# Performance work log

Hardware: AMD Instinct MI355X
Metric: run time of the kernel (lower is better)

The kernel has to match this reference:

```python
import jax, jax.numpy as jnp
import numpy as np

N = 8192        # n_nodes
NFEAT = 512
NHID = 256
AVG_DEG = 32
K = 64          # mean_kwargs k
TEMP = 1.0      # mean_kwargs temperature


def setup_inputs() -> dict:
    key = jax.random.key(0)
    ks = jax.random.split(key, 5)
    x = jax.random.normal(ks[0], (N, NFEAT), jnp.float32)
    edge_index = jax.random.randint(ks[1], (2, N * AVG_DEG), 0, N, dtype=jnp.int64)
    W1 = jax.random.normal(ks[2], (NFEAT, NHID), jnp.float32) / np.sqrt(NFEAT)
    b1 = jnp.zeros((NHID,), jnp.float32)
    W2 = jax.random.normal(ks[3], (NHID, NHID), jnp.float32) / np.sqrt(NHID)
    b2 = jnp.zeros((NHID,), jnp.float32)
    return {"x": x, "edge_index": edge_index, "W1": W1, "b1": b1, "W2": W2, "b2": b2}


def _gcn_norm(edge_index, n, dtype):
    # PyG gcn_norm: add self-loops (weight 1), deg over col, sym normalization
    loops = jnp.arange(n, dtype=edge_index.dtype)
    row = jnp.concatenate([edge_index[0], loops])
    col = jnp.concatenate([edge_index[1], loops])
    w = jnp.ones(row.shape[0], dtype)
    deg = jnp.zeros((n,), dtype).at[col].add(w)
    dis = jnp.where(deg > 0, jax.lax.rsqrt(jnp.where(deg > 0, deg, 1.0)), 0.0)
    return row, col, dis[row] * w * dis[col]


def _soft_k_medoid(row, col, w, x):
    # soft_weighted_medoid_k_neighborhood(A, x, k=K, temperature=TEMP, with_weight_correction=True)
    n, d = x.shape
    A = jnp.zeros((n, n), x.dtype).at[row, col].add(w)   # coalesced dense adjacency
    topk_a, topk_idx = jax.lax.top_k(A, K)               # [n, K] neighbor weights / ids
    xk = x[topk_idx]                                     # [n, K, d]
    sq = jnp.sum(xk * xk, axis=-1)                       # [n, K]
    G = jnp.einsum('nkd,nld->nkl', xk, xk)               # Gram per node
    d2 = jnp.maximum(sq[:, :, None] + sq[:, None, :] - 2.0 * G, 0.0)
    pos = d2 > 0
    dist = jnp.where(pos, jnp.sqrt(jnp.where(pos, d2, 1.0)), 0.0)  # safe sqrt (grad-safe)
    # weighted sum of distances to each top-k candidate j: c[n,j] = sum_l a[n,l] * ||x_l - x_j||
    c = jnp.einsum('nl,nlj->nj', topk_a, dist)
    c = jnp.where(topk_a == 0, jnp.finfo(x.dtype).max, c)
    soft = jax.nn.softmax(-c / TEMP, axis=-1)            # [n, K]
    soft = soft * topk_a                                 # with_weight_correction
    soft = soft / jnp.sum(soft, axis=-1, keepdims=True)
    row_sum = jnp.sum(A, axis=-1)                        # preserve neighborhood mass
    return row_sum[:, None] * jnp.einsum('nk,nkd->nd', soft, xk)


def reference(x, edge_index, W1, b1, W2, b2):
    n = x.shape[0]
    row, col, w = _gcn_norm(edge_index, n, x.dtype)
    h = jax.nn.relu(_soft_k_medoid(row, col, w, x @ W1) + b1)   # gc1 + relu (dropout: eval = identity)
    return jax.nn.relu(_soft_k_medoid(row, col, w, h @ W2) + b2)  # gc2 + relu
```

## Files before the change

### kernel.cpp

```cpp
#include <hip/hip_runtime.h>

typedef _Float16 half4 __attribute__((ext_vector_type(4)));
typedef _Float16 half8 __attribute__((ext_vector_type(8)));
typedef float f32x4 __attribute__((ext_vector_type(4)));

#define NNODE 8192
#define NHID  256
#define RCAP  128
#define KCAP  64

__global__ __launch_bounds__(256) void k_fused1(
    int* deg, int* rowcnt, int* flag, const void* edges,
    const float* __restrict__ W1, _Float16* __restrict__ w1T,
    const float* __restrict__ W2, _Float16* __restrict__ w2T,
    const float* __restrict__ x, _Float16* __restrict__ xh) {
    const int b = blockIdx.x, t = threadIdx.x;
    if (b < 32) {
        int i = b * 256 + t;
        deg[i] = 0; rowcnt[i] = 0;
        if (i == 0) {
            const long long* e = (const long long*)edges;
            int ok = 1;
            for (int k = 0; k < 64; ++k) { long long v = e[k]; if (v < 0 || v >= NNODE) ok = 0; }
            *flag = ok;
        }
    } else if (b < 32 + 4096) {
        int i = (b - 32) * 256 + t;
        float4 v = ((const float4*)x)[i];
        half4 h;
        h[0] = (_Float16)v.x; h[1] = (_Float16)v.y;
        h[2] = (_Float16)v.z; h[3] = (_Float16)v.w;
        *(half4*)&xh[4 * (size_t)i] = h;
    } else if (b < 32 + 4096 + 512) {
        int idx = (b - 4128) * 256 + t;
        int k = idx >> 8, n = idx & 255;
        w1T[(size_t)n * 512 + k] = (_Float16)W1[idx];
    } else {
        int idx = (b - 4640) * 256 + t;
        int k = idx >> 8, n = idx & 255;
        w2T[(size_t)n * 256 + k] = (_Float16)W2[idx];
    }
}

#define GLS 72

__device__ __forceinline__ void gemm_body(
    const _Float16* __restrict__ Ahi, const _Float16* __restrict__ BT,
    _Float16* __restrict__ Chi, int K, int bm, int bn) {
    __shared__ _Float16 sA[64][GLS];
    __shared__ _Float16 sB[64][GLS];
    const int t = threadIdx.x;
    const int lane = t & 63, L15 = lane & 15, q = lane >> 4;
    const int w = t >> 6, wr = w >> 1, wc = w & 1;
    f32x4 acc[2][2];
#pragma unroll
    for (int a = 0; a < 2; ++a)
#pragma unroll
        for (int b2 = 0; b2 < 2; ++b2) acc[a][b2] = (f32x4){0.f, 0.f, 0.f, 0.f};

    for (int k0 = 0; k0 < K; k0 += 64) {
#pragma unroll
        for (int i = 0; i < 2; ++i) {
            int row = i * 32 + (t >> 3), ch = t & 7;
            *(half8*)&sA[row][ch * 8] =
                *(const half8*)(Ahi + (size_t)(bm + row) * K + k0 + ch * 8);
            *(half8*)&sB[row][ch * 8] =
                *(const half8*)(BT + (size_t)(bn + row) * K + k0 + ch * 8);
        }
        __syncthreads();
#pragma unroll
        for (int ks = 0; ks < 2; ++ks) {
            const int ko = ks * 32 + q * 8;
            half8 ah[2], bh[2];
#pragma unroll
            for (int tr = 0; tr < 2; ++tr)
                ah[tr] = *(const half8*)&sA[32 * wr + 16 * tr + L15][ko];
#pragma unroll
            for (int tc = 0; tc < 2; ++tc)
                bh[tc] = *(const half8*)&sB[32 * wc + 16 * tc + L15][ko];
#pragma unroll
            for (int tr = 0; tr < 2; ++tr)
#pragma unroll
                for (int tc = 0; tc < 2; ++tc)
                    acc[tr][tc] = __builtin_amdgcn_mfma_f32_16x16x32_f16(ah[tr], bh[tc], acc[tr][tc], 0, 0, 0);
        }
        __syncthreads();
    }
#pragma unroll
    for (int tr = 0; tr < 2; ++tr)
#pragma unroll
        for (int tc = 0; tc < 2; ++tc)
#pragma unroll
            for (int r = 0; r < 4; ++r) {
                int rowg = bm + 32 * wr + 16 * tr + q * 4 + r;
                int colg = bn + 32 * wc + 16 * tc + L15;
                Chi[(size_t)rowg * NHID + colg] = (_Float16)acc[tr][tc][r];
            }
}

__global__ __launch_bounds__(256) void k_fused2(
    const void* edges, const int* flag, int* rowcnt, int* nbr, int* deg, int E, int nbuild,
    const _Float16* __restrict__ xh, const _Float16* __restrict__ w1T, _Float16* __restrict__ X1) {
    if ((int)blockIdx.x < nbuild) {
        int i = blockIdx.x * 256 + threadIdx.x;
        int total = E + NNODE;
        if (i >= total) return;
        int r, c;
        if (i < E) {
            if (*flag) {
                const long long* e = (const long long*)edges;
                r = (int)e[i]; c = (int)e[E + i];
            } else {
                const int* e = (const int*)edges;
                r = e[i]; c = e[E + i];
            }
        } else { r = i - E; c = r; }
        int pos = atomicAdd(&rowcnt[r], 1);
        if (pos < RCAP) nbr[r * RCAP + pos] = c;
        atomicAdd(&deg[c], 1);
    } else {
        int g = blockIdx.x - nbuild;
        gemm_body(xh, w1T, X1, 512, (g >> 2) * 64, (g & 3) * 64);
    }
}

__global__ __launch_bounds__(256) void k_gemm(
    const _Float16* __restrict__ Ahi, const _Float16* __restrict__ BT,
    _Float16* __restrict__ Chi, int K) {
    gemm_body(Ahi, BT, Chi, K, blockIdx.x * 64, blockIdx.y * 64);
}

__global__ __launch_bounds__(256) void k_dedup(const int* __restrict__ nbr,
                                               const int* __restrict__ rowcnt,
                                               const int* __restrict__ deg,
                                               int* __restrict__ cols,
                                               float* __restrict__ wout,
                                               float* __restrict__ rsum) {
    __shared__ int lc[2][RCAP];
    __shared__ float lw[2][RCAP];
    __shared__ unsigned char kp[2][RCAP];
    __shared__ int s_cw[2][2];
    __shared__ float s_rw[2][2];
    const int t = threadIdx.x;
    const int half = t >> 7, st = t & 127;
    const int wid = st >> 6, lane = t & 63;
    const int r = blockIdx.x * 2 + half;
    int n = rowcnt[r]; if (n > RCAP) n = RCAP;
    if (st < n) lc[half][st] = nbr[r * RCAP + st];
    __syncthreads();
    float dr = 1.f / sqrtf((float)deg[r]);
    bool keep = false; float wv = 0.f;
    if (st < n) {
        int c = lc[half][st];
        int mult = 0; bool first = true;
        for (int i = 0; i < n; ++i) {
            int ci = lc[half][i];
            if (ci == c) { mult++; if (i < st) first = false; }
        }
        keep = first;
        if (first) wv = (float)mult * dr * (1.f / sqrtf((float)deg[c]));
    }
    kp[half][st] = keep ? 1 : 0; lw[half][st] = wv;
    float rv = wv;
#pragma unroll
    for (int d = 1; d < 64; d <<= 1) rv += __shfl_xor(rv, d, 64);
    unsigned long long b = __ballot(keep);
    int pre = __popcll(b & ((1ull << lane) - 1ull));
    int cw = __popcll(b);
    if (lane == 0) { s_cw[half][wid] = cw; s_rw[half][wid] = rv; }
    __syncthreads();
    int total = s_cw[half][0] + s_cw[half][1];
    if (st == 0) rsum[r] = s_rw[half][0] + s_rw[half][1];
    const int base = r * KCAP;
    if (total <= KCAP) {
        int off = (wid ? s_cw[half][0] : 0) + pre;
        if (keep) { cols[base + off] = lc[half][st]; wout[base + off] = wv; }
        for (int m = total + st; m < KCAP; m += 128) { cols[base + m] = r; wout[base + m] = 0.f; }
    } else if (st == 0) {
        for (int s = 0; s < KCAP; ++s) {
            int best = -1;
            for (int i = 0; i < n; ++i) {
                if (!kp[half][i]) continue;
                if (best < 0 || lw[half][i] > lw[half][best] ||
                    (lw[half][i] == lw[half][best] && lc[half][i] < lc[half][best])) best = i;
            }
            cols[base + s] = lc[half][best]; wout[base + s] = lw[half][best]; kp[half][best] = 0;
        }
    }
}

#define SK 136

__global__ __launch_bounds__(256, 6) void k_medoid(
    const _Float16* __restrict__ Xhi,
    const float* __restrict__ bias,
    float* __restrict__ OutF, _Float16* __restrict__ OutHi,
    const int* __restrict__ cols, const float* __restrict__ wts,
    const float* __restrict__ rsum, int writeH) {
    __shared__ _Float16 sh[64][SK];
    __shared__ float s_a[64];
    __shared__ float s_sq[64];
    __shared__ float s_cpart[2][64];
    __shared__ float s_u[64];
    __shared__ int   s_cols[64];
    __shared__ float s_red[4][288];

    const int node = blockIdx.x;
    const int t = threadIdx.x;
    const int w = t >> 6, lane = t & 63;
    const int L15 = lane & 15, q = lane >> 4;
    const int wr = w >> 1, wc = w & 1;

    if (t < 64) { s_cols[t] = cols[node * KCAP + t]; s_a[t] = wts[node * KCAP + t]; }
    __syncthreads();

    f32x4 acc[2][2];
#pragma unroll
    for (int a = 0; a < 2; ++a)
#pragma unroll
        for (int b = 0; b < 2; ++b) acc[a][b] = (f32x4){0.f, 0.f, 0.f, 0.f};

    const int ch = t & 15, rr = t >> 4;
    for (int phase = 0; phase < 2; ++phase) {
#pragma unroll
        for (int i = 0; i < 4; ++i) {
            int l = i * 16 + rr;
            *(half8*)&sh[l][ch * 8] =
                *(const half8*)(Xhi + ((size_t)s_cols[l] << 8) + phase * 128 + ch * 8);
        }
        __syncthreads();
#pragma unroll
        for (int ks = 0; ks < 4; ++ks) {
            const int ko = ks * 32 + q * 8;
            half8 ah[2], bh[2];
#pragma unroll
            for (int tr = 0; tr < 2; ++tr) ah[tr] = *(const half8*)&sh[32 * wr + 16 * tr + L15][ko];
#pragma unroll
            for (int tc = 0; tc < 2; ++tc) bh[tc] = *(const half8*)&sh[32 * wc + 16 * tc + L15][ko];
#pragma unroll
            for (int tr = 0; tr < 2; ++tr)
#pragma unroll
                for (int tc = 0; tc < 2; ++tc)
                    acc[tr][tc] = __builtin_amdgcn_mfma_f32_16x16x32_f16(ah[tr], bh[tc], acc[tr][tc], 0, 0, 0);
        }
        if (phase == 0) __syncthreads();
    }

#pragma unroll
    for (int tr = 0; tr < 2; ++tr)
#pragma unroll
        for (int tc = 0; tc < 2; ++tc)
            if (32 * wr + 16 * tr == 32 * wc + 16 * tc) {
#pragma unroll
                for (int r = 0; r < 4; ++r)
                    if (L15 == q * 4 + r) s_sq[32 * wr + 16 * tr + L15] = acc[tr][tc][r];
            }
    __syncthreads();

    f32x4 sq4[2], a4[2];
#pragma unroll
    for (int tr = 0; tr < 2; ++tr) {
        sq4[tr] = *(const f32x4*)&s_sq[32 * wr + 16 * tr + 4 * q];
        a4[tr]  = *(const f32x4*)&s_a [32 * wr + 16 * tr + 4 * q];
    }
#pragma unroll
    for (int tc = 0; tc < 2; ++tc) {
        const int colg = 32 * wc + 16 * tc + L15;
        const float sqc = s_sq[colg];
        float pj = 0.f;
#pragma unroll
        for (int tr = 0; tr < 2; ++tr)
#pragma unroll
            for (int r = 0; r < 4; ++r) {
                float d2 = sq4[tr][r] + sqc - 2.f * acc[tr][tc][r];
                float dist = d2 > 0.f ? __builtin_amdgcn_sqrtf(d2) : 0.f;
                pj = fmaf(a4[tr][r], dist, pj);
            }
        pj += __shfl_xor(pj, 16, 64);
        pj += __shfl_xor(pj, 32, 64);
        if (q == 0) s_cpart[wr][colg] = pj;
    }
    __syncthreads();

    if (w == 0) {
        int j = lane;
        float c = s_cpart[0][j] + s_cpart[1][j];
        float aj = s_a[j];
        bool valid = aj > 0.f;
        float cv = valid ? c : 3.4e38f;
        float mn = cv;
#pragma unroll
        for (int d = 1; d < 64; d <<= 1) mn = fminf(mn, __shfl_xor(mn, d, 64));
        float e = valid ? __expf(mn - c) * aj : 0.f;
        float s = e;
#pragma unroll
        for (int d = 1; d < 64; d <<= 1) s += __shfl_xor(s, d, 64);
        s_u[j] = e * (rsum[node] / s);
    }
    __syncthreads();

    const int oct = t & 31, jb = t >> 5;
    float accd[8] = {0.f, 0.f, 0.f, 0.f, 0.f, 0.f, 0.f, 0.f};
#pragma unroll
    for (int jj = 0; jj < 8; ++jj) {
        int j = jb * 8 + jj;
        float u = s_u[j];
        half8 xv;
        if (oct < 16) xv = *(const half8*)(Xhi + ((size_t)s_cols[j] << 8) + oct * 8);
        else          xv = *(const half8*)&sh[j][(oct - 16) * 8];
#pragma unroll
        for (int e = 0; e < 8; ++e) accd[e] = fmaf(u, (float)xv[e], accd[e]);
    }
#pragma unroll
    for (int e = 0; e < 8; ++e) accd[e] += __shfl_xor(accd[e], 32, 64);
    if (lane < 32) {
#pragma unroll
        for (int e = 0; e < 8; ++e) s_red[w][9 * oct + e] = accd[e];
    }
    __syncthreads();
    const int idx = 9 * (t >> 3) + (t & 7);
    float o = s_red[0][idx] + s_red[1][idx] + s_red[2][idx] + s_red[3][idx];
    float res = fmaxf(o + bias[t], 0.f);
    size_t oi = (size_t)node * NHID + t;
    if (writeH) OutHi[oi] = (_Float16)res;
    else        OutF[oi] = res;
}

extern "C" void kernel_launch(void* const* d_in, const int* in_sizes, int n_in,
                              void* d_out, int out_size, void* d_ws, size_t ws_size,
                              hipStream_t stream) {
    const float* x  = (const float*)d_in[0];
    const void*  ei = d_in[1];
    const float* W1 = (const float*)d_in[2];
    const float* b1 = (const float*)d_in[3];
    const float* W2 = (const float*)d_in[4];
    const float* b2 = (const float*)d_in[5];
    float* out = (float*)d_out;
    const int E = in_sizes[1] / 2;

    char* p = (char*)d_ws;
    auto alloc = [&](size_t bytes) { char* q = p; p += (bytes + 255) & ~(size_t)255; return q; };
    int*      deg    = (int*)alloc((size_t)NNODE * 4);
    int*      rowcnt = (int*)alloc((size_t)NNODE * 4);
    int*      flag   = (int*)alloc(256);
    int*      colsA  = (int*)alloc((size_t)NNODE * KCAP * 4);
    float*    wA     = (float*)alloc((size_t)NNODE * KCAP * 4);
    float*    rsum   = (float*)alloc((size_t)NNODE * 4);
    _Float16* xh     = (_Float16*)alloc((size_t)NNODE * 512 * 2);
    _Float16* w1T    = (_Float16*)alloc((size_t)512 * NHID * 2);
    _Float16* w2T    = (_Float16*)alloc((size_t)NHID * NHID * 2);
    _Float16* X1hi   = (_Float16*)alloc((size_t)NNODE * NHID * 2);
    _Float16* Hhi    = (_Float16*)alloc((size_t)NNODE * NHID * 2);
    int*      nbr    = (int*)alloc((size_t)NNODE * RCAP * 4);

    const int nbuild = (E + NNODE + 255) / 256;

    k_fused1<<<32 + 4096 + 512 + 256, 256, 0, stream>>>(deg, rowcnt, flag, ei, W1, w1T, W2, w2T, x, xh);
    k_fused2<<<nbuild + 512, 256, 0, stream>>>(ei, flag, rowcnt, nbr, deg, E, nbuild, xh, w1T, X1hi);
    k_dedup<<<NNODE / 2, 256, 0, stream>>>(nbr, rowcnt, deg, colsA, wA, rsum);
    k_medoid<<<NNODE, 256, 0, stream>>>(X1hi, b1, nullptr, Hhi, colsA, wA, rsum, 1);
    k_gemm<<<dim3(NNODE / 64, NHID / 64), 256, 0, stream>>>(Hhi, w2T, X1hi, 256);
    k_medoid<<<NNODE, 256, 0, stream>>>(X1hi, b2, out, nullptr, colsA, wA, rsum, 0);
}
```

Before: 214.6 us.

## Merge all stages into one cooperative persistent kernel with grid syncs

```diff
diff --git a/kernel.cpp b/kernel.cpp
--- a/kernel.cpp
+++ b/kernel.cpp
@@ -1,4 +1,7 @@
 #include <hip/hip_runtime.h>
+#include <hip/hip_cooperative_groups.h>
+
+namespace cg = cooperative_groups;
 
 typedef _Float16 half4 __attribute__((ext_vector_type(4)));
 typedef _Float16 half8 __attribute__((ext_vector_type(8)));
@@ -8,47 +11,20 @@
 #define NHID  256
 #define RCAP  128
 #define KCAP  64
-
-__global__ __launch_bounds__(256) void k_fused1(
-    int* deg, int* rowcnt, int* flag, const void* edges,
-    const float* __restrict__ W1, _Float16* __restrict__ w1T,
-    const float* __restrict__ W2, _Float16* __restrict__ w2T,
-    const float* __restrict__ x, _Float16* __restrict__ xh) {
-    const int b = blockIdx.x, t = threadIdx.x;
-    if (b < 32) {
-        int i = b * 256 + t;
-        deg[i] = 0; rowcnt[i] = 0;
-        if (i == 0) {
-            const long long* e = (const long long*)edges;
-            int ok = 1;
-            for (int k = 0; k < 64; ++k) { long long v = e[k]; if (v < 0 || v >= NNODE) ok = 0; }
-            *flag = ok;
-        }
-    } else if (b < 32 + 4096) {
-        int i = (b - 32) * 256 + t;
-        float4 v = ((const float4*)x)[i];
-        half4 h;
-        h[0] = (_Float16)v.x; h[1] = (_Float16)v.y;
-        h[2] = (_Float16)v.z; h[3] = (_Float16)v.w;
-        *(half4*)&xh[4 * (size_t)i] = h;
-    } else if (b < 32 + 4096 + 512) {
-        int idx = (b - 4128) * 256 + t;
-        int k = idx >> 8, n = idx & 255;
-        w1T[(size_t)n * 512 + k] = (_Float16)W1[idx];
-    } else {
-        int idx = (b - 4640) * 256 + t;
-        int k = idx >> 8, n = idx & 255;
-        w2T[(size_t)n * 256 + k] = (_Float16)W2[idx];
-    }
-}
-
-#define GLS 72
+#define GLS   72
+#define SK    136
+
+struct SmemGemm   { _Float16 sA[64][GLS]; _Float16 sB[64][GLS]; };
+struct SmemDedup  { int lc[2][RCAP]; float lw[2][RCAP]; unsigned char kp[2][RCAP];
+                    int s_cw[2][2]; float s_rw[2][2]; };
+struct SmemMedoid { _Float16 sh[64][SK]; float s_a[64]; float s_sq[64];
+                    float s_cpart[2][64]; float s_u[64]; int s_cols[64];
+                    float s_red[4][288]; };
 
 __device__ __forceinline__ void gemm_body(
-    const _Float16* __restrict__ Ahi, const _Float16* __restrict__ BT,
+    char* smraw, const _Float16* __restrict__ Ahi, const _Float16* __restrict__ BT,
     _Float16* __restrict__ Chi, int K, int bm, int bn) {
-    __shared__ _Float16 sA[64][GLS];
-    __shared__ _Float16 sB[64][GLS];
+    SmemGemm& sm = *(SmemGemm*)smraw;
     const int t = threadIdx.x;
     const int lane = t & 63, L15 = lane & 15, q = lane >> 4;
     const int w = t >> 6, wr = w >> 1, wc = w & 1;
@@ -62,9 +38,9 @@
 #pragma unroll
         for (int i = 0; i < 2; ++i) {
             int row = i * 32 + (t >> 3), ch = t & 7;
-            *(half8*)&sA[row][ch * 8] =
+            *(half8*)&sm.sA[row][ch * 8] =
                 *(const half8*)(Ahi + (size_t)(bm + row) * K + k0 + ch * 8);
-            *(half8*)&sB[row][ch * 8] =
+            *(half8*)&sm.sB[row][ch * 8] =
                 *(const half8*)(BT + (size_t)(bn + row) * K + k0 + ch * 8);
         }
         __syncthreads();
@@ -74,10 +50,10 @@
             half8 ah[2], bh[2];
 #pragma unroll
             for (int tr = 0; tr < 2; ++tr)
-                ah[tr] = *(const half8*)&sA[32 * wr + 16 * tr + L15][ko];
+                ah[tr] = *(const half8*)&sm.sA[32 * wr + 16 * tr + L15][ko];
 #pragma unroll
             for (int tc = 0; tc < 2; ++tc)
-                bh[tc] = *(const half8*)&sB[32 * wc + 16 * tc + L15][ko];
+                bh[tc] = *(const half8*)&sm.sB[32 * wc + 16 * tc + L15][ko];
 #pragma unroll
             for (int tr = 0; tr < 2; ++tr)
 #pragma unroll
@@ -98,120 +74,72 @@
             }
 }
 
-__global__ __launch_bounds__(256) void k_fused2(
-    const void* edges, const int* flag, int* rowcnt, int* nbr, int* deg, int E, int nbuild,
-    const _Float16* __restrict__ xh, const _Float16* __restrict__ w1T, _Float16* __restrict__ X1) {
-    if ((int)blockIdx.x < nbuild) {
-        int i = blockIdx.x * 256 + threadIdx.x;
-        int total = E + NNODE;
-        if (i >= total) return;
-        int r, c;
-        if (i < E) {
-            if (*flag) {
-                const long long* e = (const long long*)edges;
-                r = (int)e[i]; c = (int)e[E + i];
-            } else {
-                const int* e = (const int*)edges;
-                r = e[i]; c = e[E + i];
-            }
-        } else { r = i - E; c = r; }
-        int pos = atomicAdd(&rowcnt[r], 1);
-        if (pos < RCAP) nbr[r * RCAP + pos] = c;
-        atomicAdd(&deg[c], 1);
-    } else {
-        int g = blockIdx.x - nbuild;
-        gemm_body(xh, w1T, X1, 512, (g >> 2) * 64, (g & 3) * 64);
-    }
-}
-
-__global__ __launch_bounds__(256) void k_gemm(
-    const _Float16* __restrict__ Ahi, const _Float16* __restrict__ BT,
-    _Float16* __restrict__ Chi, int K) {
-    gemm_body(Ahi, BT, Chi, K, blockIdx.x * 64, blockIdx.y * 64);
-}
-
-__global__ __launch_bounds__(256) void k_dedup(const int* __restrict__ nbr,
-                                               const int* __restrict__ rowcnt,
-                                               const int* __restrict__ deg,
-                                               int* __restrict__ cols,
-                                               float* __restrict__ wout,
-                                               float* __restrict__ rsum) {
-    __shared__ int lc[2][RCAP];
-    __shared__ float lw[2][RCAP];
-    __shared__ unsigned char kp[2][RCAP];
-    __shared__ int s_cw[2][2];
-    __shared__ float s_rw[2][2];
+__device__ __forceinline__ void dedup_body(
+    char* smraw, const int* __restrict__ nbr, const int* __restrict__ rowcnt,
+    const int* __restrict__ deg, int* __restrict__ cols, float* __restrict__ wout,
+    float* __restrict__ rsum, int grp) {
+    SmemDedup& sm = *(SmemDedup*)smraw;
     const int t = threadIdx.x;
     const int half = t >> 7, st = t & 127;
     const int wid = st >> 6, lane = t & 63;
-    const int r = blockIdx.x * 2 + half;
+    const int r = grp * 2 + half;
     int n = rowcnt[r]; if (n > RCAP) n = RCAP;
-    if (st < n) lc[half][st] = nbr[r * RCAP + st];
+    if (st < n) sm.lc[half][st] = nbr[r * RCAP + st];
     __syncthreads();
     float dr = 1.f / sqrtf((float)deg[r]);
     bool keep = false; float wv = 0.f;
     if (st < n) {
-        int c = lc[half][st];
+        int c = sm.lc[half][st];
         int mult = 0; bool first = true;
         for (int i = 0; i < n; ++i) {
-            int ci = lc[half][i];
+            int ci = sm.lc[half][i];
             if (ci == c) { mult++; if (i < st) first = false; }
         }
         keep = first;
         if (first) wv = (float)mult * dr * (1.f / sqrtf((float)deg[c]));
     }
-    kp[half][st] = keep ? 1 : 0; lw[half][st] = wv;
+    sm.kp[half][st] = keep ? 1 : 0; sm.lw[half][st] = wv;
     float rv = wv;
 #pragma unroll
     for (int d = 1; d < 64; d <<= 1) rv += __shfl_xor(rv, d, 64);
     unsigned long long b = __ballot(keep);
     int pre = __popcll(b & ((1ull << lane) - 1ull));
     int cw = __popcll(b);
-    if (lane == 0) { s_cw[half][wid] = cw; s_rw[half][wid] = rv; }
-    __syncthreads();
-    int total = s_cw[half][0] + s_cw[half][1];
-    if (st == 0) rsum[r] = s_rw[half][0] + s_rw[half][1];
+    if (lane == 0) { sm.s_cw[half][wid] = cw; sm.s_rw[half][wid] = rv; }
+    __syncthreads();
+    int total = sm.s_cw[half][0] + sm.s_cw[half][1];
+    if (st == 0) rsum[r] = sm.s_rw[half][0] + sm.s_rw[half][1];
     const int base = r * KCAP;
     if (total <= KCAP) {
-        int off = (wid ? s_cw[half][0] : 0) + pre;
-        if (keep) { cols[base + off] = lc[half][st]; wout[base + off] = wv; }
+        int off = (wid ? sm.s_cw[half][0] : 0) + pre;
+        if (keep) { cols[base + off] = sm.lc[half][st]; wout[base + off] = wv; }
         for (int m = total + st; m < KCAP; m += 128) { cols[base + m] = r; wout[base + m] = 0.f; }
     } else if (st == 0) {
         for (int s = 0; s < KCAP; ++s) {
             int best = -1;
             for (int i = 0; i < n; ++i) {
-                if (!kp[half][i]) continue;
-                if (best < 0 || lw[half][i] > lw[half][best] ||
-                    (lw[half][i] == lw[half][best] && lc[half][i] < lc[half][best])) best = i;
+                if (!sm.kp[half][i]) continue;
+                if (best < 0 || sm.lw[half][i] > sm.lw[half][best] ||
+                    (sm.lw[half][i] == sm.lw[half][best] && sm.lc[half][i] < sm.lc[half][best])) best = i;
             }
-            cols[base + s] = lc[half][best]; wout[base + s] = lw[half][best]; kp[half][best] = 0;
-        }
-    }
-}
-
-#define SK 136
-
-__global__ __launch_bounds__(256, 6) void k_medoid(
-    const _Float16* __restrict__ Xhi,
-    const float* __restrict__ bias,
+            cols[base + s] = sm.lc[half][best]; wout[base + s] = sm.lw[half][best]; sm.kp[half][best] = 0;
+        }
+    }
+    __syncthreads();
+}
+
+__device__ __forceinline__ void medoid_body(
+    char* smraw, const _Float16* __restrict__ Xhi, const float* __restrict__ bias,
     float* __restrict__ OutF, _Float16* __restrict__ OutHi,
     const int* __restrict__ cols, const float* __restrict__ wts,
-    const float* __restrict__ rsum, int writeH) {
-    __shared__ _Float16 sh[64][SK];
-    __shared__ float s_a[64];
-    __shared__ float s_sq[64];
-    __shared__ float s_cpart[2][64];
-    __shared__ float s_u[64];
-    __shared__ int   s_cols[64];
-    __shared__ float s_red[4][288];
-
-    const int node = blockIdx.x;
+    const float* __restrict__ rsum, int node, int writeH) {
+    SmemMedoid& sm = *(SmemMedoid*)smraw;
     const int t = threadIdx.x;
     const int w = t >> 6, lane = t & 63;
     const int L15 = lane & 15, q = lane >> 4;
     const int wr = w >> 1, wc = w & 1;
 
-    if (t < 64) { s_cols[t] = cols[node * KCAP + t]; s_a[t] = wts[node * KCAP + t]; }
+    if (t < 64) { sm.s_cols[t] = cols[node * KCAP + t]; sm.s_a[t] = wts[node * KCAP + t]; }
     __syncthreads();
 
     f32x4 acc[2][2];
@@ -225,8 +153,8 @@
 #pragma unroll
         for (int i = 0; i < 4; ++i) {
             int l = i * 16 + rr;
-            *(half8*)&sh[l][ch * 8] =
-                *(const half8*)(Xhi + ((size_t)s_cols[l] << 8) + phase * 128 + ch * 8);
+            *(half8*)&sm.sh[l][ch * 8] =
+                *(const half8*)(Xhi + ((size_t)sm.s_cols[l] << 8) + phase * 128 + ch * 8);
         }
         __syncthreads();
 #pragma unroll
@@ -234,9 +162,9 @@
             const int ko = ks * 32 + q * 8;
             half8 ah[2], bh[2];
 #pragma unroll
-            for (int tr = 0; tr < 2; ++tr) ah[tr] = *(const half8*)&sh[32 * wr + 16 * tr + L15][ko];
-#pragma unroll
-            for (int tc = 0; tc < 2; ++tc) bh[tc] = *(const half8*)&sh[32 * wc + 16 * tc + L15][ko];
+            for (int tr = 0; tr < 2; ++tr) ah[tr] = *(const half8*)&sm.sh[32 * wr + 16 * tr + L15][ko];
+#pragma unroll
+            for (int tc = 0; tc < 2; ++tc) bh[tc] = *(const half8*)&sm.sh[32 * wc + 16 * tc + L15][ko];
 #pragma unroll
             for (int tr = 0; tr < 2; ++tr)
 #pragma unroll
@@ -253,20 +181,20 @@
             if (32 * wr + 16 * tr == 32 * wc + 16 * tc) {
 #pragma unroll
                 for (int r = 0; r < 4; ++r)
-                    if (L15 == q * 4 + r) s_sq[32 * wr + 16 * tr + L15] = acc[tr][tc][r];
+                    if (L15 == q * 4 + r) sm.s_sq[32 * wr + 16 * tr + L15] = acc[tr][tc][r];
             }
     __syncthreads();
 
     f32x4 sq4[2], a4[2];
 #pragma unroll
     for (int tr = 0; tr < 2; ++tr) {
-        sq4[tr] = *(const f32x4*)&s_sq[32 * wr + 16 * tr + 4 * q];
-        a4[tr]  = *(const f32x4*)&s_a [32 * wr + 16 * tr + 4 * q];
+        sq4[tr] = *(const f32x4*)&sm.s_sq[32 * wr + 16 * tr + 4 * q];
+        a4[tr]  = *(const f32x4*)&sm.s_a [32 * wr + 16 * tr + 4 * q];
     }
 #pragma unroll
     for (int tc = 0; tc < 2; ++tc) {
         const int colg = 32 * wc + 16 * tc + L15;
-        const float sqc = s_sq[colg];
+        const float sqc = sm.s_sq[colg];
         float pj = 0.f;
 #pragma unroll
         for (int tr = 0; tr < 2; ++tr)
@@ -278,14 +206,14 @@
             }
         pj += __shfl_xor(pj, 16, 64);
         pj += __shfl_xor(pj, 32, 64);
-        if (q == 0) s_cpart[wr][colg] = pj;
+        if (q == 0) sm.s_cpart[wr][colg] = pj;
     }
     __syncthreads();
 
     if (w == 0) {
         int j = lane;
-        float c = s_cpart[0][j] + s_cpart[1][j];
-        float aj = s_a[j];
+        float c = sm.s_cpart[0][j] + sm.s_cpart[1][j];
+        float aj = sm.s_a[j];
         bool valid = aj > 0.f;
         float cv = valid ? c : 3.4e38f;
         float mn = cv;
@@ -295,7 +223,7 @@
         float s = e;
 #pragma unroll
         for (int d = 1; d < 64; d <<= 1) s += __shfl_xor(s, d, 64);
-        s_u[j] = e * (rsum[node] / s);
+        sm.s_u[j] = e * (rsum[node] / s);
     }
     __syncthreads();
 
@@ -304,10 +232,10 @@
 #pragma unroll
     for (int jj = 0; jj < 8; ++jj) {
         int j = jb * 8 + jj;
-        float u = s_u[j];
+        float u = sm.s_u[j];
         half8 xv;
-        if (oct < 16) xv = *(const half8*)(Xhi + ((size_t)s_cols[j] << 8) + oct * 8);
-        else          xv = *(const half8*)&sh[j][(oct - 16) * 8];
+        if (oct < 16) xv = *(const half8*)(Xhi + ((size_t)sm.s_cols[j] << 8) + oct * 8);
+        else          xv = *(const half8*)&sm.sh[j][(oct - 16) * 8];
 #pragma unroll
         for (int e = 0; e < 8; ++e) accd[e] = fmaf(u, (float)xv[e], accd[e]);
     }
@@ -315,15 +243,147 @@
     for (int e = 0; e < 8; ++e) accd[e] += __shfl_xor(accd[e], 32, 64);
     if (lane < 32) {
 #pragma unroll
-        for (int e = 0; e < 8; ++e) s_red[w][9 * oct + e] = accd[e];
+        for (int e = 0; e < 8; ++e) sm.s_red[w][9 * oct + e] = accd[e];
     }
     __syncthreads();
     const int idx = 9 * (t >> 3) + (t & 7);
-    float o = s_red[0][idx] + s_red[1][idx] + s_red[2][idx] + s_red[3][idx];
+    float o = sm.s_red[0][idx] + sm.s_red[1][idx] + sm.s_red[2][idx] + sm.s_red[3][idx];
     float res = fmaxf(o + bias[t], 0.f);
     size_t oi = (size_t)node * NHID + t;
     if (writeH) OutHi[oi] = (_Float16)res;
     else        OutF[oi] = res;
+}
+
+__device__ __forceinline__ void stage_prep(
+    int gid, int nthr, int bid, int t,
+    int* deg, int* rowcnt, int* flag, const void* edges,
+    const float* __restrict__ x, _Float16* __restrict__ xh,
+    const float* __restrict__ W1, _Float16* __restrict__ w1T,
+    const float* __restrict__ W2, _Float16* __restrict__ w2T) {
+    for (int i = gid; i < NNODE; i += nthr) { deg[i] = 0; rowcnt[i] = 0; }
+    if (bid == 0 && t < 64) {
+        const long long* e = (const long long*)edges;
+        long long v = e[t];
+        unsigned long long bad = __ballot(v < 0 || v >= (long long)NNODE);
+        if (t == 0) *flag = (bad == 0) ? 1 : 0;
+    }
+    for (int i = gid; i < NNODE * 512 / 4; i += nthr) {
+        float4 v = ((const float4*)x)[i];
+        half4 h;
+        h[0] = (_Float16)v.x; h[1] = (_Float16)v.y;
+        h[2] = (_Float16)v.z; h[3] = (_Float16)v.w;
+        *(half4*)&xh[4 * (size_t)i] = h;
+    }
+    for (int i = gid; i < 512 * NHID; i += nthr) {
+        int k = i >> 8, n = i & 255;
+        w1T[(size_t)n * 512 + k] = (_Float16)W1[i];
+    }
+    for (int i = gid; i < NHID * NHID; i += nthr) {
+        int k = i >> 8, n = i & 255;
+        w2T[(size_t)n * 256 + k] = (_Float16)W2[i];
+    }
+}
+
+__device__ __forceinline__ void stage_s1(
+    char* smem, int bid, int nb, int t,
+    const void* edges, const int* flag, int* rowcnt, int* nbr, int* deg, int E,
+    const _Float16* __restrict__ xh, const _Float16* __restrict__ w1T, _Float16* __restrict__ X1) {
+    const int ng = nb >> 1;
+    if (bid < ng) {
+        for (int g = bid; g < 512; g += ng)
+            gemm_body(smem, xh, w1T, X1, 512, (g >> 2) * 64, (g & 3) * 64);
+    } else {
+        const int ns = nb - ng;
+        const int fl = *flag;
+        const int total = E + NNODE;
+        for (int i = (bid - ng) * 256 + t; i < total; i += ns * 256) {
+            int r, c;
+            if (i < E) {
+                if (fl) {
+                    const long long* e = (const long long*)edges;
+                    r = (int)e[i]; c = (int)e[E + i];
+                } else {
+                    const int* e = (const int*)edges;
+                    r = e[i]; c = e[E + i];
+                }
+            } else { r = i - E; c = r; }
+            int pos = atomicAdd(&rowcnt[r], 1);
+            if (pos < RCAP) nbr[r * RCAP + pos] = c;
+            atomicAdd(&deg[c], 1);
+        }
+    }
+}
+
+__global__ __launch_bounds__(256, 4) void k_mega(
+    const float* __restrict__ x, const void* edges,
+    const float* __restrict__ W1, const float* __restrict__ b1,
+    const float* __restrict__ W2, const float* __restrict__ b2,
+    float* __restrict__ out,
+    int* deg, int* rowcnt, int* flag, int* nbr, int* cols, float* wA,
+    float* rsum, _Float16* xh, _Float16* w1T, _Float16* w2T,
+    _Float16* X1, _Float16* Hh, int E) {
+    cg::grid_group grid = cg::this_grid();
+    __shared__ __align__(16) char smem[sizeof(SmemMedoid)];
+    const int nb = gridDim.x, bid = blockIdx.x, t = threadIdx.x;
+    const int gid = bid * 256 + t, nthr = nb * 256;
+
+    stage_prep(gid, nthr, bid, t, deg, rowcnt, flag, edges, x, xh, W1, w1T, W2, w2T);
+    grid.sync();
+    stage_s1(smem, bid, nb, t, edges, flag, rowcnt, nbr, deg, E, xh, w1T, X1);
+    grid.sync();
+    for (int g = bid; g < NNODE / 2; g += nb)
+        dedup_body(smem, nbr, rowcnt, deg, cols, wA, rsum, g);
+    grid.sync();
+    for (int node = bid; node < NNODE; node += nb)
+        medoid_body(smem, X1, b1, nullptr, Hh, cols, wA, rsum, node, 1);
+    grid.sync();
+    for (int g = bid; g < 512; g += nb)
+        gemm_body(smem, Hh, w2T, X1, 256, (g >> 2) * 64, (g & 3) * 64);
+    grid.sync();
+    for (int node = bid; node < NNODE; node += nb)
+        medoid_body(smem, X1, b2, out, nullptr, cols, wA, rsum, node, 0);
+}
+
+__global__ __launch_bounds__(256) void fb_prep(
+    int* deg, int* rowcnt, int* flag, const void* edges,
+    const float* __restrict__ x, _Float16* __restrict__ xh,
+    const float* __restrict__ W1, _Float16* __restrict__ w1T,
+    const float* __restrict__ W2, _Float16* __restrict__ w2T) {
+    stage_prep(blockIdx.x * 256 + threadIdx.x, gridDim.x * 256, blockIdx.x, threadIdx.x,
+               deg, rowcnt, flag, edges, x, xh, W1, w1T, W2, w2T);
+}
+
+__global__ __launch_bounds__(256) void fb_s1(
+    const void* edges, const int* flag, int* rowcnt, int* nbr, int* deg, int E,
+    const _Float16* __restrict__ xh, const _Float16* __restrict__ w1T, _Float16* __restrict__ X1) {
+    __shared__ __align__(16) char smem[sizeof(SmemGemm)];
+    stage_s1(smem, blockIdx.x, gridDim.x, threadIdx.x, edges, flag, rowcnt, nbr, deg, E, xh, w1T, X1);
+}
+
+__global__ __launch_bounds__(256) void fb_dedup(
+    const int* __restrict__ nbr, const int* __restrict__ rowcnt, const int* __restrict__ deg,
+    int* __restrict__ cols, float* __restrict__ wout, float* __restrict__ rsum) {
+    __shared__ __align__(16) char smem[sizeof(SmemDedup)];
+    for (int g = blockIdx.x; g < NNODE / 2; g += gridDim.x)
+        dedup_body(smem, nbr, rowcnt, deg, cols, wout, rsum, g);
+}
+
+__global__ __launch_bounds__(256, 4) void fb_medoid(
+    const _Float16* __restrict__ Xhi, const float* __restrict__ bias,
+    float* __restrict__ OutF, _Float16* __restrict__ OutHi,
+    const int* __restrict__ cols, const float* __restrict__ wts,
+    const float* __restrict__ rsum, int writeH) {
+    __shared__ __align__(16) char smem[sizeof(SmemMedoid)];
+    for (int node = blockIdx.x; node < NNODE; node += gridDim.x)
+        medoid_body(smem, Xhi, bias, OutF, OutHi, cols, wts, rsum, node, writeH);
+}
+
+__global__ __launch_bounds__(256) void fb_gemm(
+    const _Float16* __restrict__ Ahi, const _Float16* __restrict__ BT,
+    _Float16* __restrict__ Chi, int K) {
+    __shared__ __align__(16) char smem[sizeof(SmemGemm)];
+    for (int g = blockIdx.x; g < 512; g += gridDim.x)
+        gemm_body(smem, Ahi, BT, Chi, K, (g >> 2) * 64, (g & 3) * 64);
 }
 
 extern "C" void kernel_launch(void* const* d_in, const int* in_sizes, int n_in,
@@ -336,7 +396,7 @@
     const float* W2 = (const float*)d_in[4];
     const float* b2 = (const float*)d_in[5];
     float* out = (float*)d_out;
-    const int E = in_sizes[1] / 2;
+    int E = in_sizes[1] / 2;
 
     char* p = (char*)d_ws;
     auto alloc = [&](size_t bytes) { char* q = p; p += (bytes + 255) & ~(size_t)255; return q; };
@@ -349,16 +409,41 @@
     _Float16* xh     = (_Float16*)alloc((size_t)NNODE * 512 * 2);
     _Float16* w1T    = (_Float16*)alloc((size_t)512 * NHID * 2);
     _Float16* w2T    = (_Float16*)alloc((size_t)NHID * NHID * 2);
-    _Float16* X1hi   = (_Float16*)alloc((size_t)NNODE * NHID * 2);
-    _Float16* Hhi    = (_Float16*)alloc((size_t)NNODE * NHID * 2);
+    _Float16* X1     = (_Float16*)alloc((size_t)NNODE * NHID * 2);
+    _Float16* Hh     = (_Float16*)alloc((size_t)NNODE * NHID * 2);
     int*      nbr    = (int*)alloc((size_t)NNODE * RCAP * 4);
 
-    const int nbuild = (E + NNODE + 255) / 256;
-
-    k_fused1<<<32 + 4096 + 512 + 256, 256, 0, stream>>>(deg, rowcnt, flag, ei, W1, w1T, W2, w2T, x, xh);
-    k_fused2<<<nbuild + 512, 256, 0, stream>>>(ei, flag, rowcnt, nbr, deg, E, nbuild, xh, w1T, X1hi);
-    k_dedup<<<NNODE / 2, 256, 0, stream>>>(nbr, rowcnt, deg, colsA, wA, rsum);
-    k_medoid<<<NNODE, 256, 0, stream>>>(X1hi, b1, nullptr, Hhi, colsA, wA, rsum, 1);
-    k_gemm<<<dim3(NNODE / 64, NHID / 64), 256, 0, stream>>>(Hhi, w2T, X1hi, 256);
-    k_medoid<<<NNODE, 256, 0, stream>>>(X1hi, b2, out, nullptr, colsA, wA, rsum, 0);
-}
+    int dev = 0; hipGetDevice(&dev);
+    int coopAttr = 0;
+    hipDeviceGetAttribute(&coopAttr, hipDeviceAttributeCooperativeLaunch, dev);
+    int ncu = 0;
+    hipDeviceGetAttribute(&ncu, hipDeviceAttributeMultiprocessorCount, dev);
+    if (ncu <= 0) ncu = 256;
+    int maxb = 0;
+    hipError_t qe = hipOccupancyMaxActiveBlocksPerMultiprocessor(
+        &maxb, (const void*)k_mega, 256, 0);
+
+    hipError_t le = hipErrorUnknown;
+    if (coopAttr != 0 && qe == hipSuccess && maxb >= 1) {
+        int nblk = maxb * ncu;
+        if (nblk > 2048) nblk = 2048;
+        if (nblk >= 64) {
+            void* args[] = {
+                (void*)&x, (void*)&ei, (void*)&W1, (void*)&b1, (void*)&W2, (void*)&b2,
+                (void*)&out, (void*)&deg, (void*)&rowcnt, (void*)&flag, (void*)&nbr,
+                (void*)&colsA, (void*)&wA, (void*)&rsum, (void*)&xh, (void*)&w1T,
+                (void*)&w2T, (void*)&X1, (void*)&Hh, (void*)&E
+            };
+            le = hipLaunchCooperativeKernel((const void*)k_mega, dim3(nblk), dim3(256),
+                                            args, 0, stream);
+        }
+    }
+    if (le != hipSuccess) {
+        fb_prep<<<1024, 256, 0, stream>>>(deg, rowcnt, flag, ei, x, xh, W1, w1T, W2, w2T);
+        fb_s1<<<1024, 256, 0, stream>>>(ei, flag, rowcnt, nbr, deg, E, xh, w1T, X1);
+        fb_dedup<<<NNODE / 2, 256, 0, stream>>>(nbr, rowcnt, deg, colsA, wA, rsum);
+        fb_medoid<<<NNODE, 256, 0, stream>>>(X1, b1, nullptr, Hh, colsA, wA, rsum, 1);
+        fb_gemm<<<512, 256, 0, stream>>>(Hh, w2T, X1, 256);
+        fb_medoid<<<NNODE, 256, 0, stream>>>(X1, b2, out, nullptr, colsA, wA, rsum, 0);
+    }
+}
```

Measured after the change: 599.4 us. 2.79x slower.
